# Optimization experiments

Measured on AMD Instinct MI355X. Metric: run time of the kernel, lower is better.

## Reference

```python
import jax, jax.numpy as jnp
import numpy as np

B, T, C = 4, 2048, 1024
N_HEADS = 16
HEAD_DIM = C // N_HEADS


def rotary_embedding(seq_len, dim, dtype=jnp.float32):
    pos = jnp.arange(seq_len, dtype=dtype)[:, None]
    i = jnp.arange(0, dim, 2, dtype=dtype)[None, :]
    theta = pos / jnp.power(10000.0, i / dim)
    return jnp.cos(theta), jnp.sin(theta)


def apply_rotary(x, cos, sin):
    # x: [B, T, H, D]; cos/sin: [T, D//2]
    d = x.shape[-1]
    x1, x2 = x[..., : d // 2], x[..., d // 2 :]
    rotated = jnp.concatenate([-x2, x1], axis=-1)
    cos = jnp.concatenate([cos, cos], axis=-1)[None, :, None, :]
    sin = jnp.concatenate([sin, sin], axis=-1)[None, :, None, :]
    return x * cos + rotated * sin


def setup_inputs() -> dict:
    key = jax.random.key(0)
    k1, k2, k3 = jax.random.split(key, 3)
    x = jax.random.normal(k1, (B, T, C), dtype=jnp.float32)
    # lecun_normal-ish init scale
    w_qkv = jax.random.normal(k2, (C, 3 * C), dtype=jnp.float32) / np.sqrt(C)
    w_out = jax.random.normal(k3, (C, C), dtype=jnp.float32) / np.sqrt(C)
    return {"x": x, "w_qkv": w_qkv, "w_out": w_out}


def reference(x, w_qkv, w_out):
    b, t, c = x.shape
    qkv = jnp.einsum("btc,cd->btd", x, w_qkv)
    q, k, v = jnp.split(qkv, 3, axis=-1)
    q = q.reshape(b, t, N_HEADS, HEAD_DIM)
    k = k.reshape(b, t, N_HEADS, HEAD_DIM)
    v = v.reshape(b, t, N_HEADS, HEAD_DIM)
    cos, sin = rotary_embedding(t, HEAD_DIM, dtype=x.dtype)
    q = apply_rotary(q, cos, sin)
    k = apply_rotary(k, cos, sin)
    scale = jnp.sqrt(jnp.asarray(HEAD_DIM, dtype=x.dtype))
    # scores: [B, H, T, T]
    attn = jnp.einsum("bqhd,bkhd->bhqk", q, k) / scale
    mask = jnp.tril(jnp.ones((t, t), dtype=jnp.bool_))
    attn = jnp.where(mask[None, None, :, :], attn, jnp.asarray(-1e9, dtype=x.dtype))
    attn = jax.nn.softmax(attn, axis=-1)
    out = jnp.einsum("bhqk,bkhd->bqhd", attn, v).reshape(b, t, c)
    return jnp.einsum("btc,cd->btd", out, w_out)
```

## Files before the change

kernel.cpp:

```cpp
#include <hip/hip_runtime.h>
#include <stdint.h>

#define DEVI __device__ __forceinline__

typedef unsigned short ushort_t;
typedef __bf16 bf16x8 __attribute__((ext_vector_type(8)));
typedef float f32x4 __attribute__((ext_vector_type(4)));
typedef unsigned short ushort8 __attribute__((ext_vector_type(8)));
typedef short s16x4 __attribute__((ext_vector_type(4)));

#define BB 4
#define TT 2048
#define CC 1024
#define NH 16
#define HD 64
#define MM (BB*TT)

DEVI ushort_t f2bf(float f) {
    __bf16 h = (__bf16)f;
    return __builtin_bit_cast(ushort_t, h);
}

typedef const __attribute__((address_space(1))) unsigned int guint_t;
typedef __attribute__((address_space(3))) unsigned int luint_t;

DEVI void gl2lds16(const void* g, void* lds) {
    __builtin_amdgcn_global_load_lds((guint_t*)(uintptr_t)g,
                                     (luint_t*)(unsigned int)(uintptr_t)lds,
                                     16, 0, 0);
}

template <int N> DEVI void waitvm() {
    static_assert(N == 0 || N == 6, "unsupported vmcnt literal");
    if constexpr (N == 0)      asm volatile("s_waitcnt vmcnt(0)" ::: "memory");
    else if constexpr (N == 6) asm volatile("s_waitcnt vmcnt(6)" ::: "memory");
}

#define BARF() do { asm volatile("" ::: "memory"); \
                    __builtin_amdgcn_s_barrier(); \
                    asm volatile("" ::: "memory"); } while (0)
#define LGK0() asm volatile("s_waitcnt lgkmcnt(0)" ::: "memory")

__global__ void cvt_f32_bf16(const float* __restrict__ in,
                             ushort_t* __restrict__ out) {
    int i = blockIdx.x * 256 + threadIdx.x;
    const float4* p = (const float4*)in + (size_t)i * 2;
    float4 a = p[0], b = p[1];
    ushort8 r;
    r[0] = f2bf(a.x); r[1] = f2bf(a.y); r[2] = f2bf(a.z); r[3] = f2bf(a.w);
    r[4] = f2bf(b.x); r[5] = f2bf(b.y); r[6] = f2bf(b.z); r[7] = f2bf(b.w);
    *(ushort8*)(out + (size_t)i * 8) = r;
}

__global__ void transpose_f2b(const float* __restrict__ in,
                              ushort_t* __restrict__ out, int R, int Cc) {
    __shared__ ushort_t tile[32][33];
    int bx = blockIdx.x * 32;
    int by = blockIdx.y * 32;
    int tx = threadIdx.x & 31, ty = threadIdx.x >> 5;
    #pragma unroll
    for (int i = 0; i < 4; i++) {
        int r = ty * 4 + i;
        tile[r][tx] = f2bf(in[(size_t)(by + r) * Cc + bx + tx]);
    }
    __syncthreads();
    #pragma unroll
    for (int i = 0; i < 4; i++) {
        int r = ty * 4 + i;
        out[(size_t)(bx + r) * R + by + tx] = tile[tx][r];
    }
}

__global__ void rope_table(float2* __restrict__ tab) {
    int i = blockIdx.x * 256 + threadIdx.x;
    int t = i >> 5, j = i & 31;
    float inv = exp2f((float)j * -0.41524101186092029f);
    float theta = (float)t * inv;
    float s, c;
    sincosf(theta, &s, &c);
    tab[i] = make_float2(c, s);
}

__global__ void vtrans(const ushort_t* __restrict__ Vb,
                       ushort_t* __restrict__ VbT) {
    __shared__ ushort_t tile[64 * 72];
    const int bh = blockIdx.y;
    const int t0 = blockIdx.x * 64;
    const int tid = threadIdx.x;
    const int r = tid >> 2, c = (tid & 3) * 16;
    const size_t base = (size_t)bh * (TT * HD);
    const ushort_t* g = Vb + base + (size_t)(t0 + r) * HD + c;
    *(ushort8*)&tile[r * 72 + c]     = *(const ushort8*)g;
    *(ushort8*)&tile[r * 72 + c + 8] = *(const ushort8*)(g + 8);
    __syncthreads();
    ushort8 a, b;
    #pragma unroll
    for (int j = 0; j < 8; j++) a[j] = tile[(c + j) * 72 + r];
    #pragma unroll
    for (int j = 0; j < 8; j++) b[j] = tile[(c + 8 + j) * 72 + r];
    ushort_t* o = VbT + base + (size_t)r * TT + t0 + c;
    *(ushort8*)o = a;
    *(ushort8*)(o + 8) = b;
}

template <int MODE>
__global__ __launch_bounds__(512, 2) void gemm_bt(
    const ushort_t* __restrict__ A, const ushort_t* __restrict__ Bt,
    float* __restrict__ CoutF,
    ushort_t* __restrict__ Qb, ushort_t* __restrict__ Kb, ushort_t* __restrict__ Vb,
    const float2* __restrict__ rope, int M, int N, int Kd) {
    constexpr int NK = CC / 64;
    (void)M;

    __shared__ __attribute__((aligned(16))) ushort_t As[2][128 * 64];
    __shared__ __attribute__((aligned(16))) ushort_t Bs[2][256 * 64];

    const int tid = threadIdx.x;
    const int w = tid >> 6, l = tid & 63;
    const int lane15 = l & 15, quad = l >> 4;
    const int wm = (w >> 2) * 64;
    const int wn = (w & 3) * 64;

    const int nbn = gridDim.x;
    const int nwg = nbn * gridDim.y;
    const int lid = blockIdx.y * nbn + blockIdx.x;
    const int sid = (lid & 7) * (nwg >> 3) + (lid >> 3);
    const int bn = sid % nbn, bm = sid / nbn;

    const int sr = tid >> 3;
    const int sc = tid & 7;
    const int srcswz = (sc ^ (sr & 7)) * 16;

    auto stA = [&](int buf, int t, int ln) {
        int gr = bm * 128 + ln * 64 + sr;
        size_t e;
        if constexpr (MODE == 2)
            e = (size_t)(gr >> 11) * 2097152 + (size_t)t * 131072
                + (size_t)(gr & (TT - 1)) * 64;
        else
            e = (size_t)gr * (size_t)Kd + (size_t)t * 64;
        gl2lds16((const char*)(A + e) + srcswz,
                 (char*)&As[buf][0] + ln * 8192 + tid * 16);
    };
    auto stB = [&](int buf, int t, int ln) {
        int gr = bn * 256 + ln * 64 + sr;
        size_t e = (size_t)gr * (size_t)Kd + (size_t)t * 64;
        gl2lds16((const char*)(Bt + e) + srcswz,
                 (char*)&Bs[buf][0] + ln * 8192 + tid * 16);
    };

    f32x4 acc[4][4];
    #pragma unroll
    for (int m = 0; m < 4; ++m)
        #pragma unroll
        for (int n = 0; n < 4; ++n)
            acc[m][n] = f32x4{0.f, 0.f, 0.f, 0.f};

    stA(0, 0, 0); stA(0, 0, 1);
    stB(0, 0, 0); stB(0, 0, 1); stB(0, 0, 2); stB(0, 0, 3);
    waitvm<0>();
    BARF();

    const int swz = (lane15 & 7) << 4;
    bf16x8 aR[2][2];
    bf16x8 bR[2][2][2];

#define LDA_SET(P, MH)                                                        \
    { _Pragma("unroll") for (int i = 0; i < 2; ++i)                           \
      _Pragma("unroll") for (int kk = 0; kk < 2; ++kk)                        \
        aR[i][kk] = *(const bf16x8*)((const char*)&As[P][0] +                 \
            (wm + MH * 32 + i * 16 + lane15) * 128 +                          \
            ((kk * 64 + quad * 16) ^ swz)); }

#define LDB_SET(P, NH)                                                        \
    { _Pragma("unroll") for (int j = 0; j < 2; ++j)                           \
      _Pragma("unroll") for (int kk = 0; kk < 2; ++kk)                        \
        bR[NH][j][kk] = *(const bf16x8*)((const char*)&Bs[P][0] +             \
            (wn + (NH * 2 + j) * 16 + lane15) * 128 +                         \
            ((kk * 64 + quad * 16) ^ swz)); }

#define MFMA_Q(MH, NH)                                                        \
    { __builtin_amdgcn_s_setprio(1);                                          \
      _Pragma("unroll") for (int kk = 0; kk < 2; ++kk)                        \
      _Pragma("unroll") for (int i = 0; i < 2; ++i)                           \
      _Pragma("unroll") for (int j = 0; j < 2; ++j)                           \
        acc[MH * 2 + i][NH * 2 + j] =                                         \
            __builtin_amdgcn_mfma_f32_16x16x32_bf16(                          \
                aR[i][kk], bR[NH][j][kk], acc[MH * 2 + i][NH * 2 + j],        \
                0, 0, 0);                                                     \
      __builtin_amdgcn_s_setprio(0); }

    for (int t = 0; t < NK; ++t) {
        const int p = t & 1;
        const bool st1 = (t + 1 < NK);
        LDA_SET(p, 0);
        LDB_SET(p, 0);
        if (st1) { stA(p ^ 1, t + 1, 0); stA(p ^ 1, t + 1, 1); }
        BARF(); LGK0();
        MFMA_Q(0, 0);
        BARF();
        LDB_SET(p, 1);
        if (st1) { stB(p ^ 1, t + 1, 0); stB(p ^ 1, t + 1, 1); }
        BARF(); LGK0();
        MFMA_Q(0, 1);
        BARF();
        LDA_SET(p, 1);
        if (st1) { stB(p ^ 1, t + 1, 2); stB(p ^ 1, t + 1, 3); }
        BARF(); LGK0();
        MFMA_Q(1, 1);
        BARF();
        if (t + 2 < NK) {
            stA(p, t + 2, 0); stA(p, t + 2, 1);
            stB(p, t + 2, 0); stB(p, t + 2, 1);
            stB(p, t + 2, 2); stB(p, t + 2, 3);
        }
        MFMA_Q(1, 0);
        if (st1) {
            if (t + 2 < NK) waitvm<6>();
            else            waitvm<0>();
            BARF();
        }
    }
#undef LDA_SET
#undef LDB_SET
#undef MFMA_Q

    if constexpr (MODE == 1) {
        const float SCQ = 0.125f * 1.4426950408889634f;
        const int colbase = bn * 256 + wn;
        const int seg = colbase >> 10;
        const int h = (colbase & 1023) >> 6;
        #pragma unroll
        for (int m = 0; m < 4; ++m) {
            int row0 = bm * 128 + wm + m * 16 + quad * 4;
            #pragma unroll
            for (int r = 0; r < 4; ++r) {
                int row = row0 + r;
                int b = row >> 11, t = row & (TT - 1);
                size_t ob = ((size_t)(b * NH + h) * TT + t) * HD;
                if (seg == 2) {
                    #pragma unroll
                    for (int n = 0; n < 4; ++n)
                        Vb[ob + n * 16 + lane15] = f2bf(acc[m][n][r]);
                } else {
                    ushort_t* dst = (seg == 0) ? Qb : Kb;
                    #pragma unroll
                    for (int n = 0; n < 2; ++n) {
                        int j = n * 16 + lane15;
                        float2 cs = rope[t * 32 + j];
                        float x1 = acc[m][n][r];
                        float x2 = acc[m][n + 2][r];
                        float y1 = x1 * cs.x - x2 * cs.y;
                        float y2 = x2 * cs.x + x1 * cs.y;
                        if (seg == 0) { y1 *= SCQ; y2 *= SCQ; }
                        dst[ob + j]      = f2bf(y1);
                        dst[ob + 32 + j] = f2bf(y2);
                    }
                }
            }
        }
    } else {
        #pragma unroll
        for (int m = 0; m < 4; ++m) {
            #pragma unroll
            for (int r = 0; r < 4; ++r) {
                size_t rb = (size_t)(bm * 128 + wm + m * 16 + quad * 4 + r) * N
                            + bn * 256 + wn;
                #pragma unroll
                for (int n = 0; n < 4; ++n)
                    CoutF[rb + n * 16 + lane15] = acc[m][n][r];
            }
        }
    }
}

__global__ __launch_bounds__(512, 4) void attn_kernel(
    ushort_t* __restrict__ Qb, const ushort_t* __restrict__ Kb,
    const ushort_t* __restrict__ VbT) {
    __shared__ __attribute__((aligned(16))) ushort_t Ks[2][64 * 72];
    __shared__ __attribute__((aligned(16))) ushort_t Vs[2][64 * 72];

    const int tid = threadIdx.x;
    const int w = tid >> 6, l = tid & 63;
    const int lane15 = l & 15, quad = l >> 4;

    const int d = blockIdx.y * gridDim.x + blockIdx.x;
    const int xcd = d & 7, j = d >> 3;
    const int bh = xcd * 8 + (j & 7);
    const int qt = (int)((0x765489AB3210CDEFull >> (4 * (j >> 3))) & 15);
    const size_t base = (size_t)bh * (TT * HD);

    const int sr = tid >> 3;
    const int sd = (tid & 7) * 8;
    const ushort_t* kgb = Kb  + base + (size_t)sr * HD + sd;
    const ushort_t* vgb = VbT + base + (size_t)sr * TT + sd;

    const int q0 = qt * 128;
    const int rbase = q0 + w * 16;
    const int ktmax = 2 * qt + 1;

    bf16x8 qf0, qf1;
    {
        const ushort_t* qp = Qb + base + (size_t)(rbase + lane15) * HD + quad * 8;
        qf0 = *(const bf16x8*)qp;
        qf1 = *(const bf16x8*)(qp + 32);
    }

    f32x4 o[4];
    #pragma unroll
    for (int nt = 0; nt < 4; nt++) o[nt] = f32x4{0.f, 0.f, 0.f, 0.f};
    f32x4 lacc = f32x4{0.f, 0.f, 0.f, 0.f};
    float mrow = -INFINITY;

    const s16x4 ONES = {(short)0x3F80, (short)0x3F80,
                        (short)0x3F80, (short)0x3F80};

    ushort8 kr = *(const ushort8*)kgb;
    ushort8 vr = *(const ushort8*)vgb;
    *(ushort8*)&Ks[0][sr * 72 + sd] = kr;
    *(ushort8*)&Vs[0][sr * 72 + sd] = vr;
    kr = *(const ushort8*)(kgb + (size_t)64 * HD);
    vr = *(const ushort8*)(vgb + 64);
    __syncthreads();

    for (int kt = 0; kt <= ktmax; kt++) {
        const int buf = kt & 1;
        if (kt < ktmax) {
            *(ushort8*)&Ks[buf ^ 1][sr * 72 + sd] = kr;
            *(ushort8*)&Vs[buf ^ 1][sr * 72 + sd] = vr;
        }
        if (kt + 2 <= ktmax) {
            kr = *(const ushort8*)(kgb + (size_t)(kt + 2) * 64 * HD);
            vr = *(const ushort8*)(vgb + (size_t)(kt + 2) * 64);
        }

        if (kt * 64 <= rbase + 15) {
            f32x4 s[4];
            #pragma unroll
            for (int c = 0; c < 4; c++) {
                bf16x8 k0 = *(const bf16x8*)&Ks[buf][(c * 16 + lane15) * 72 + quad * 8];
                bf16x8 k1 = *(const bf16x8*)&Ks[buf][(c * 16 + lane15) * 72 + 32 + quad * 8];
                f32x4 z = f32x4{0.f, 0.f, 0.f, 0.f};
                z = __builtin_amdgcn_mfma_f32_16x16x32_bf16(k0, qf0, z, 0, 0, 0);
                s[c] = __builtin_amdgcn_mfma_f32_16x16x32_bf16(k1, qf1, z, 0, 0, 0);
            }

            const int qrow = rbase + lane15;
            if (kt * 64 + 63 > rbase) {
                #pragma unroll
                for (int c = 0; c < 4; c++)
                    #pragma unroll
                    for (int r = 0; r < 4; r++)
                        if (kt * 64 + c * 16 + quad * 4 + r > qrow) s[c][r] = -1e9f;
            }

            float a0 = fmaxf(fmaxf(s[0][0], s[0][1]), s[0][2]);
            float a1 = fmaxf(fmaxf(s[0][3], s[1][0]), s[1][1]);
            float a2 = fmaxf(fmaxf(s[1][2], s[1][3]), s[2][0]);
            float a3 = fmaxf(fmaxf(s[2][1], s[2][2]), s[2][3]);
            float a4 = fmaxf(fmaxf(s[3][0], s[3][1]), s[3][2]);
            float mt = fmaxf(fmaxf(a0, a1), a2);
            mt = fmaxf(fmaxf(mt, a3), fmaxf(a4, s[3][3]));

            if (!__all(mt - mrow <= 8.0f)) {
                float mf = fmaxf(mt, __shfl_xor(mt, 16, 64));
                mf = fmaxf(mf, __shfl_xor(mf, 32, 64));
                float mn = fmaxf(mrow, mf);
                float alpha = __builtin_amdgcn_exp2f(mrow - mn);
                mrow = mn;
                #pragma unroll
                for (int r = 0; r < 4; r++) {
                    float aO = __shfl(alpha, quad * 4 + r, 64);
                    #pragma unroll
                    for (int nt = 0; nt < 4; nt++) o[nt][r] *= aO;
                    lacc[r] *= aO;
                }
            }

            #pragma unroll
            for (int c = 0; c < 4; c++) {
                s16x4 pf;
                #pragma unroll
                for (int r = 0; r < 4; r++)
                    pf[r] = (short)f2bf(__builtin_amdgcn_exp2f(s[c][r] - mrow));
                lacc = __builtin_amdgcn_mfma_f32_16x16x16bf16_1k(
                    pf, ONES, lacc, 0, 0, 0);
                #pragma unroll
                for (int nt = 0; nt < 4; nt++) {
                    s16x4 vf = *(const s16x4*)&Vs[buf][(nt * 16 + lane15) * 72 +
                                                      c * 16 + quad * 4];
                    o[nt] = __builtin_amdgcn_mfma_f32_16x16x16bf16_1k(
                        pf, vf, o[nt], 0, 0, 0);
                }
            }
        }

        if (kt < ktmax) __syncthreads();
    }

    #pragma unroll
    for (int r = 0; r < 4; r++) {
        float lO = 1.0f / lacc[r];
        size_t rb = base + (size_t)(rbase + quad * 4 + r) * HD;
        #pragma unroll
        for (int nt = 0; nt < 4; nt++)
            Qb[rb + nt * 16 + lane15] = f2bf(o[nt][r] * lO);
    }
}

extern "C" void kernel_launch(void* const* d_in, const int* in_sizes, int n_in,
                              void* d_out, int out_size, void* d_ws, size_t ws_size,
                              hipStream_t stream) {
    const float* x    = (const float*)d_in[0];
    const float* wqkv = (const float*)d_in[1];
    const float* wout = (const float*)d_in[2];
    float* out = (float*)d_out;

    char* ws = (char*)d_ws;
    ushort_t* WqkvT = (ushort_t*)(ws);
    ushort_t* WoutT = (ushort_t*)(ws + 6291456);
    float2*   rope  = (float2*)  (ws + 8388608);
    ushort_t* Xb    = (ushort_t*)(ws + 8912896);
    ushort_t* Qb    = (ushort_t*)(ws + 8912896 + 16777216);
    ushort_t* Kb    = (ushort_t*)(ws + 8912896 + 2 * 16777216);
    ushort_t* Vb    = (ushort_t*)(ws + 8912896 + 3 * 16777216);
    ushort_t* VbT   = Xb;

    cvt_f32_bf16<<<dim3(MM * CC / (256 * 8)), 256, 0, stream>>>(x, Xb);
    transpose_f2b<<<dim3(3 * CC / 32, CC / 32), 256, 0, stream>>>(wqkv, WqkvT, CC, 3 * CC);
    transpose_f2b<<<dim3(CC / 32, CC / 32), 256, 0, stream>>>(wout, WoutT, CC, CC);
    rope_table<<<dim3(256), 256, 0, stream>>>(rope);

    gemm_bt<1><<<dim3(3 * CC / 256, MM / 128), 512, 0, stream>>>(
        Xb, WqkvT, nullptr, Qb, Kb, Vb, rope, MM, 3 * CC, CC);

    vtrans<<<dim3(TT / 64, BB * NH), 256, 0, stream>>>(Vb, VbT);

    attn_kernel<<<dim3(16, BB * NH), 512, 0, stream>>>(Qb, Kb, VbT);

    gemm_bt<2><<<dim3(CC / 256, MM / 128), 512, 0, stream>>>(
        Qb, WoutT, out, nullptr, nullptr, nullptr, nullptr, MM, CC, CC);
}
```

Before: 275.6 us.

## Enlarge GEMM block tile to 256x256 and restage A/B prefetch pipeline

Doubles the M dimension of the GEMM block tile from 128 to 256 rows, so each wave now owns a 128x64 output tile with twice as many accumulators. Each B tile is then reused across more rows of A, which cuts global and LDS traffic per FLOP. The prefetch schedule is also reorganised: A is loaded one stage ahead into the other buffer, and B two stages ahead into the current buffer, with the vmcnt wait adjusted to match. In exchange, LDS use doubles, leaving roughly one block per CU, and the grids shrink (384 blocks for QKV, 128 for the output projection), which risks poor CU occupancy and wave quantisation on the smaller GEMM.

```diff
diff --git a/kernel.cpp b/kernel.cpp
--- a/kernel.cpp
+++ b/kernel.cpp
@@ -31,9 +31,9 @@
 }
 
 template <int N> DEVI void waitvm() {
-    static_assert(N == 0 || N == 6, "unsupported vmcnt literal");
+    static_assert(N == 0 || N == 4, "unsupported vmcnt literal");
     if constexpr (N == 0)      asm volatile("s_waitcnt vmcnt(0)" ::: "memory");
-    else if constexpr (N == 6) asm volatile("s_waitcnt vmcnt(6)" ::: "memory");
+    else if constexpr (N == 4) asm volatile("s_waitcnt vmcnt(4)" ::: "memory");
 }
 
 #define BARF() do { asm volatile("" ::: "memory"); \
@@ -112,13 +112,13 @@
     constexpr int NK = CC / 64;
     (void)M;
 
-    __shared__ __attribute__((aligned(16))) ushort_t As[2][128 * 64];
+    __shared__ __attribute__((aligned(16))) ushort_t As[2][256 * 64];
     __shared__ __attribute__((aligned(16))) ushort_t Bs[2][256 * 64];
 
     const int tid = threadIdx.x;
     const int w = tid >> 6, l = tid & 63;
     const int lane15 = l & 15, quad = l >> 4;
-    const int wm = (w >> 2) * 64;
+    const int wm = (w >> 2) * 128;
     const int wn = (w & 3) * 64;
 
     const int nbn = gridDim.x;
@@ -132,7 +132,7 @@
     const int srcswz = (sc ^ (sr & 7)) * 16;
 
     auto stA = [&](int buf, int t, int ln) {
-        int gr = bm * 128 + ln * 64 + sr;
+        int gr = bm * 256 + ln * 64 + sr;
         size_t e;
         if constexpr (MODE == 2)
             e = (size_t)(gr >> 11) * 2097152 + (size_t)t * 131072
@@ -149,80 +149,77 @@
                  (char*)&Bs[buf][0] + ln * 8192 + tid * 16);
     };
 
-    f32x4 acc[4][4];
-    #pragma unroll
-    for (int m = 0; m < 4; ++m)
+    f32x4 acc[8][4];
+    #pragma unroll
+    for (int m = 0; m < 8; ++m)
         #pragma unroll
         for (int n = 0; n < 4; ++n)
             acc[m][n] = f32x4{0.f, 0.f, 0.f, 0.f};
 
-    stA(0, 0, 0); stA(0, 0, 1);
+    stA(0, 0, 0); stA(0, 0, 1); stA(0, 0, 2); stA(0, 0, 3);
     stB(0, 0, 0); stB(0, 0, 1); stB(0, 0, 2); stB(0, 0, 3);
-    waitvm<0>();
+    stB(1, 1, 0); stB(1, 1, 1); stB(1, 1, 2); stB(1, 1, 3);
+    waitvm<4>();
     BARF();
 
     const int swz = (lane15 & 7) << 4;
-    bf16x8 aR[2][2];
-    bf16x8 bR[2][2][2];
-
-#define LDA_SET(P, MH)                                                        \
-    { _Pragma("unroll") for (int i = 0; i < 2; ++i)                           \
+    bf16x8 aR[4][2];
+    bf16x8 bR[4][2];
+
+#define LDA_H(P, MH)                                                          \
+    { _Pragma("unroll") for (int i = 0; i < 4; ++i)                           \
       _Pragma("unroll") for (int kk = 0; kk < 2; ++kk)                        \
         aR[i][kk] = *(const bf16x8*)((const char*)&As[P][0] +                 \
-            (wm + MH * 32 + i * 16 + lane15) * 128 +                          \
+            (wm + MH * 64 + i * 16 + lane15) * 128 +                          \
             ((kk * 64 + quad * 16) ^ swz)); }
 
-#define LDB_SET(P, NH)                                                        \
+#define LDB_H(P, NHF)                                                         \
     { _Pragma("unroll") for (int j = 0; j < 2; ++j)                           \
       _Pragma("unroll") for (int kk = 0; kk < 2; ++kk)                        \
-        bR[NH][j][kk] = *(const bf16x8*)((const char*)&Bs[P][0] +             \
-            (wn + (NH * 2 + j) * 16 + lane15) * 128 +                         \
+        bR[NHF * 2 + j][kk] = *(const bf16x8*)((const char*)&Bs[P][0] +       \
+            (wn + (NHF * 2 + j) * 16 + lane15) * 128 +                        \
             ((kk * 64 + quad * 16) ^ swz)); }
 
-#define MFMA_Q(MH, NH)                                                        \
+#define MFMA_Q(MH, NHF)                                                       \
     { __builtin_amdgcn_s_setprio(1);                                          \
       _Pragma("unroll") for (int kk = 0; kk < 2; ++kk)                        \
-      _Pragma("unroll") for (int i = 0; i < 2; ++i)                           \
+      _Pragma("unroll") for (int i = 0; i < 4; ++i)                           \
       _Pragma("unroll") for (int j = 0; j < 2; ++j)                           \
-        acc[MH * 2 + i][NH * 2 + j] =                                         \
+        acc[MH * 4 + i][NHF * 2 + j] =                                        \
             __builtin_amdgcn_mfma_f32_16x16x32_bf16(                          \
-                aR[i][kk], bR[NH][j][kk], acc[MH * 2 + i][NH * 2 + j],        \
+                aR[i][kk], bR[NHF * 2 + j][kk], acc[MH * 4 + i][NHF * 2 + j], \
                 0, 0, 0);                                                     \
       __builtin_amdgcn_s_setprio(0); }
 
     for (int t = 0; t < NK; ++t) {
         const int p = t & 1;
-        const bool st1 = (t + 1 < NK);
-        LDA_SET(p, 0);
-        LDB_SET(p, 0);
-        if (st1) { stA(p ^ 1, t + 1, 0); stA(p ^ 1, t + 1, 1); }
+        const bool s1 = (t + 1 < NK), s2 = (t + 2 < NK);
+        LDA_H(p, 0);
+        LDB_H(p, 0);
+        if (s1) { stA(p ^ 1, t + 1, 0); stA(p ^ 1, t + 1, 1); }
         BARF(); LGK0();
         MFMA_Q(0, 0);
         BARF();
-        LDB_SET(p, 1);
-        if (st1) { stB(p ^ 1, t + 1, 0); stB(p ^ 1, t + 1, 1); }
+        LDB_H(p, 1);
+        if (s1) { stA(p ^ 1, t + 1, 2); stA(p ^ 1, t + 1, 3); }
         BARF(); LGK0();
         MFMA_Q(0, 1);
         BARF();
-        LDA_SET(p, 1);
-        if (st1) { stB(p ^ 1, t + 1, 2); stB(p ^ 1, t + 1, 3); }
+        LDA_H(p, 1);
+        if (s2) { stB(p, t + 2, 0); stB(p, t + 2, 1); }
         BARF(); LGK0();
         MFMA_Q(1, 1);
         BARF();
-        if (t + 2 < NK) {
-            stA(p, t + 2, 0); stA(p, t + 2, 1);
-            stB(p, t + 2, 0); stB(p, t + 2, 1);
-            stB(p, t + 2, 2); stB(p, t + 2, 3);
-        }
+        if (s2) { stB(p, t + 2, 2); stB(p, t + 2, 3); }
         MFMA_Q(1, 0);
-        if (st1) {
-            if (t + 2 < NK) waitvm<6>();
-            else            waitvm<0>();
+        if (s1) {
+            if (s2) waitvm<4>();
+            else    waitvm<0>();
             BARF();
         }
     }
-#undef LDA_SET
-#undef LDB_SET
+#undef LDA_H
+#undef LDB_H
 #undef MFMA_Q
 
     if constexpr (MODE == 1) {
@@ -231,8 +228,8 @@
         const int seg = colbase >> 10;
         const int h = (colbase & 1023) >> 6;
         #pragma unroll
-        for (int m = 0; m < 4; ++m) {
-            int row0 = bm * 128 + wm + m * 16 + quad * 4;
+        for (int m = 0; m < 8; ++m) {
+            int row0 = bm * 256 + wm + m * 16 + quad * 4;
             #pragma unroll
             for (int r = 0; r < 4; ++r) {
                 int row = row0 + r;
@@ -261,10 +258,10 @@
         }
     } else {
         #pragma unroll
-        for (int m = 0; m < 4; ++m) {
+        for (int m = 0; m < 8; ++m) {
             #pragma unroll
             for (int r = 0; r < 4; ++r) {
-                size_t rb = (size_t)(bm * 128 + wm + m * 16 + quad * 4 + r) * N
+                size_t rb = (size_t)(bm * 256 + wm + m * 16 + quad * 4 + r) * N
                             + bn * 256 + wn;
                 #pragma unroll
                 for (int n = 0; n < 4; ++n)
@@ -431,13 +428,13 @@
     transpose_f2b<<<dim3(CC / 32, CC / 32), 256, 0, stream>>>(wout, WoutT, CC, CC);
     rope_table<<<dim3(256), 256, 0, stream>>>(rope);
 
-    gemm_bt<1><<<dim3(3 * CC / 256, MM / 128), 512, 0, stream>>>(
+    gemm_bt<1><<<dim3(3 * CC / 256, MM / 256), 512, 0, stream>>>(
         Xb, WqkvT, nullptr, Qb, Kb, Vb, rope, MM, 3 * CC, CC);
 
     vtrans<<<dim3(TT / 64, BB * NH), 256, 0, stream>>>(Vb, VbT);
 
     attn_kernel<<<dim3(16, BB * NH), 512, 0, stream>>>(Qb, Kb, VbT);
 
-    gemm_bt<2><<<dim3(CC / 256, MM / 128), 512, 0, stream>>>(
+    gemm_bt<2><<<dim3(CC / 256, MM / 256), 512, 0, stream>>>(
         Qb, WoutT, out, nullptr, nullptr, nullptr, nullptr, MM, CC, CC);
 }
```

Result: faster. 269.7 us (-2.1%).
